# Performance work log

Measured on AMD Instinct MI355X. Metric: run time of the kernel, lower is better.

The kernel has to match this reference:

```python
import jax, jax.numpy as jnp
import numpy as np

K = 3          # deformable conv kernel size
DG = 4         # deformable groups
PAD = (K - 1) // 2


def _deform_conv(x, offset, w, dg=DG, pad=PAD):
    """DCNv1 forward (stride=1, dilation=1, conv groups=1, no bias).

    x:      [B, C, H, W]
    offset: [B, dg*K*K*2, H, W]  layout per group: (dy, dx) per kernel tap
    w:      [O, C, K, K]
    """
    B, C, H, W = x.shape
    O = w.shape[0]
    k2 = K * K
    gC = C // dg

    off = offset.reshape(B, dg, k2, 2, H, W)
    dy, dx = off[:, :, :, 0], off[:, :, :, 1]          # [B, dg, k2, H, W]

    ky, kx = jnp.meshgrid(jnp.arange(K), jnp.arange(K), indexing='ij')
    ky = ky.reshape(k2).astype(x.dtype)
    kx = kx.reshape(k2).astype(x.dtype)
    hi = jnp.arange(H, dtype=x.dtype)
    wi = jnp.arange(W, dtype=x.dtype)

    # absolute fractional sample coords: p0 - pad + kernel tap + learned offset
    ys = hi[None, None, None, :, None] - pad + ky[None, None, :, None, None] + dy
    xs = wi[None, None, None, None, :] - pad + kx[None, None, :, None, None] + dx

    y0 = jnp.floor(ys)
    x0 = jnp.floor(xs)
    ly = ys - y0   # bilinear weights
    lx = xs - x0
    y0 = y0.astype(jnp.int32)
    x0 = x0.astype(jnp.int32)

    xg = x.reshape(B, dg, gC, H * W)

    def gather(yi, xi):
        # zero padding outside the image (per-corner validity, matches mmcv)
        valid = ((yi >= 0) & (yi < H) & (xi >= 0) & (xi < W)).astype(x.dtype)
        idx = (jnp.clip(yi, 0, H - 1) * W + jnp.clip(xi, 0, W - 1)).reshape(B, dg, -1)
        vals = jax.vmap(jax.vmap(lambda t, i: t[:, i]))(xg, idx)  # [B,dg,gC,k2*H*W]
        return vals.reshape(B, dg, gC, k2, H, W) * valid[:, :, None]

    # bilinear interpolation of the 4 corners
    sampled = ((1 - ly) * (1 - lx))[:, :, None] * gather(y0,     x0) \
            + ((1 - ly) * lx      )[:, :, None] * gather(y0,     x0 + 1) \
            + (ly       * (1 - lx))[:, :, None] * gather(y0 + 1, x0) \
            + (ly       * lx      )[:, :, None] * gather(y0 + 1, x0 + 1)
    # sampled: [B, dg, gC, k2, H, W]

    wr = w.reshape(O, dg, gC, k2)
    return jnp.einsum('bgckhw,ogck->bohw', sampled, wr)


def setup_inputs() -> dict:
    key = jax.random.key(0)
    k0, k1, k2k, k3 = jax.random.split(key, 4)
    B, C, H, W, O = 2, 256, 128, 128, 256
    oc = DG * K * K * 2
    x = jax.random.normal(k0, (B, C, H, W), jnp.float32)
    # offset conv is zero-init in the module; use small random values so the
    # deformable sampling path is actually exercised
    w_offset = jax.random.normal(k1, (oc, C, 1, 1), jnp.float32) * 0.01
    b_offset = jax.random.normal(k2k, (oc,), jnp.float32) * 0.01
    w_deform = jax.random.normal(k3, (O, C, K, K), jnp.float32) / np.sqrt(C * K * K)
    return {"x": x, "w_offset": w_offset, "b_offset": b_offset, "w_deform": w_deform}


def reference(x, w_offset, b_offset, w_deform):
    # 1x1 conv predicting offsets
    offset = jnp.einsum('bchw,oc->bohw', x, w_offset[:, :, 0, 0]) \
             + b_offset[None, :, None, None]
    # deformable conv + ReLU
    return jax.nn.relu(_deform_conv(x, offset, w_deform))
```

## Files before the change

kernel.cpp:

```cpp
#include <hip/hip_runtime.h>

#define HW 16384

typedef __attribute__((ext_vector_type(4))) float f32x4;
typedef __attribute__((ext_vector_type(8))) short bf16x8;
typedef __attribute__((ext_vector_type(4))) int i32x4;

static __device__ __forceinline__ float bf2f(short s) {
    return __uint_as_float(((unsigned)(unsigned short)s) << 16);
}
static __device__ __forceinline__ unsigned short f2bf(float f) {
    unsigned u = __float_as_uint(f);
    unsigned r = u + 0x7fffu + ((u >> 16) & 1u);
    return (unsigned short)(r >> 16);
}
static __device__ __forceinline__ int cvt_pk_bf16(float lo, float hi) {
    int r;
    asm("v_cvt_pk_bf16_f32 %0, %1, %2" : "=v"(r) : "v"(lo), "v"(hi));
    return r;
}

__global__ __launch_bounds__(256) void prep_kernel(
    const float* __restrict__ x, const float* __restrict__ wd,
    const float* __restrict__ woff,
    unsigned short* __restrict__ xT, unsigned short* __restrict__ Wc2,
    unsigned short* __restrict__ Wo2)
{
    int bid = blockIdx.x;
    int tid = threadIdx.x;
    if (bid < 2048) {
        __shared__ float tl[64][65];
        int ct = bid & 3, pt = (bid >> 2) & 255, b = bid >> 10;
        const float* xb = x + ((size_t)(b * 256 + ct * 64)) * HW + pt * 64;
        #pragma unroll
        for (int j = 0; j < 4; ++j) {
            int slot = tid + j * 256;
            int c = slot >> 4, p4 = slot & 15;
            float4 v = *(const float4*)(xb + (size_t)c * HW + p4 * 4);
            tl[c][p4 * 4 + 0] = v.x;
            tl[c][p4 * 4 + 1] = v.y;
            tl[c][p4 * 4 + 2] = v.z;
            tl[c][p4 * 4 + 3] = v.w;
        }
        __syncthreads();
        unsigned short* ob = xT + ((size_t)(b * HW + pt * 64)) * 256 + ct * 64;
        #pragma unroll
        for (int j2 = 0; j2 < 2; ++j2) {
            int slot = tid + j2 * 256;
            int p = slot >> 3, sl = slot & 7;
            i32x4 st;
            #pragma unroll
            for (int kq = 0; kq < 4; ++kq)
                ((int*)&st)[kq] = cvt_pk_bf16(tl[sl*8 + kq*2][p], tl[sl*8 + kq*2 + 1][p]);
            *(i32x4*)(ob + (size_t)p * 256 + sl * 8) = st;
        }
    } else if (bid < 2336) {
        int slot = (bid - 2048) * 256 + tid;
        int l  = slot & 63;
        int ks = (slot >> 6) & 1;
        int mi = (slot >> 7) & 3;
        int q4 = (slot >> 9) & 3;
        int kc = slot >> 11;
        int g = kc / 9, tap = kc - g * 9;
        int o = q4 * 64 + mi * 16 + (l & 15);
        int cgb = (ks * 4 + (l >> 4)) * 8;
        unsigned short* dst = Wc2 + (size_t)slot * 8;
        const float* src = wd + (size_t)o * 2304 + tap;
        #pragma unroll
        for (int e = 0; e < 8; ++e)
            dst[e] = f2bf(src[(size_t)(g * 64 + cgb + e) * 9]);
    } else {
        int slot = (bid - 2336) * 256 + tid;
        int kk = slot / 320;
        int rem = slot - kk * 320;
        int o = rem >> 2, jq = rem & 3;
        unsigned short* dst = Wo2 + (size_t)slot * 8;
        #pragma unroll
        for (int e = 0; e < 8; ++e)
            dst[e] = (o < 72) ? f2bf(woff[(size_t)o * 256 + kk * 32 + jq * 8 + e]) : (unsigned short)0;
    }
}

__global__ __launch_bounds__(512, 4) void deform_kernel(
    const unsigned short* __restrict__ xT, const unsigned short* __restrict__ Wc2,
    const unsigned short* __restrict__ Wo2, const float* __restrict__ b_off,
    float* __restrict__ out)
{
    __shared__ int   c_yx[2304];
    __shared__ float c_ly[2304];
    __shared__ float c_lx[2304];
    __shared__ __align__(16) short Sbuf[2][4096];

    const int t    = threadIdx.x;
    const int lane = t & 63;
    const int q    = t >> 6;
    const int lr   = lane & 15, lq = lane >> 4;
    int bid = blockIdx.x;
    bid = (bid & 7) * 64 + (bid >> 3);
    const int gp0  = bid << 6;
    const int b    = gp0 >> 14;
    const int hw0  = gp0 & 16383;
    const int h    = hw0 >> 7;
    const int w0   = hw0 & 127;

    {
        const int p16 = (q & 3) * 16;
        bf16x8 xv[8];
        const unsigned short* xrow = xT + ((size_t)(b * HW + hw0 + p16 + lr)) * 256 + lq * 8;
        #pragma unroll
        for (int kk = 0; kk < 8; ++kk)
            xv[kk] = *(const bf16x8*)(xrow + kk * 32);
        const int mi0 = (q < 4) ? 0 : 3;
        const int nmi = (q < 4) ? 3 : 2;
        for (int im = 0; im < nmi; ++im) {
            int mi = mi0 + im;
            f32x4 oa = (f32x4)0.f;
            #pragma unroll
            for (int kk = 0; kk < 8; ++kk) {
                bf16x8 af = *(const bf16x8*)(Wo2 + (size_t)((kk * 80 + mi * 16 + lr) * 32 + lq * 8));
                oa = __builtin_amdgcn_mfma_f32_16x16x32_bf16(af, xv[kk], oa, 0, 0, 0);
            }
            #pragma unroll
            for (int ri = 0; ri < 2; ++ri) {
                int gt = mi * 8 + lq * 2 + ri;
                if (gt < 36) {
                    int p = p16 + lr;
                    float dy = oa[ri * 2]     + b_off[2 * gt];
                    float dx = oa[ri * 2 + 1] + b_off[2 * gt + 1];
                    int tap = gt % 9;
                    float ys = (float)(h - 1 + tap / 3) + dy;
                    float xs = (float)(w0 + p - 1 + tap % 3) + dx;
                    float fy = floorf(ys), fx = floorf(xs);
                    c_yx[gt * 64 + p] = ((int)fy & 0xffff) | ((int)fx << 16);
                    c_ly[gt * 64 + p] = ys - fy;
                    c_lx[gt * 64 + p] = xs - fx;
                }
            }
        }
    }
    __syncthreads();

    f32x4 acc[2][4];
    #pragma unroll
    for (int mi = 0; mi < 2; ++mi)
        #pragma unroll
        for (int nj = 0; nj < 4; ++nj)
            acc[mi][nj] = (f32x4)0.f;

    const unsigned short* xbase = xT + ((size_t)b * HW) * 256;
    const int ppix = q * 8 + (lane >> 3);
    const int sl   = lane & 7;
    const int q4   = q >> 1;
    const int mo   = (q & 1) * 2;

    {
        int idx = ppix;
        int yx = c_yx[idx];
        int y0 = (int)(short)(yx & 0xffff);
        int x0 = yx >> 16;
        float ly = c_ly[idx], lx = c_lx[idx];
        float omy = 1.f - ly, omx = 1.f - lx;
        float vy0 = ((unsigned)y0       < 128u) ? 1.f : 0.f;
        float vy1 = ((unsigned)(y0 + 1) < 128u) ? 1.f : 0.f;
        float vx0 = ((unsigned)x0       < 128u) ? 1.f : 0.f;
        float vx1 = ((unsigned)(x0 + 1) < 128u) ? 1.f : 0.f;
        float w00 = omy * omx * vy0 * vx0, w01 = omy * lx * vy0 * vx1;
        float w10 = ly  * omx * vy1 * vx0, w11 = ly  * lx * vy1 * vx1;
        int y0c = min(max(y0, 0), 127), y1c = min(max(y0 + 1, 0), 127);
        int x0c = min(max(x0, 0), 127), x1c = min(max(x0 + 1, 0), 127);
        const unsigned short* cb = xbase + (size_t)(sl * 8);
        bf16x8 v00 = *(const bf16x8*)(cb + (size_t)(y0c * 128 + x0c) * 256);
        bf16x8 v01 = *(const bf16x8*)(cb + (size_t)(y0c * 128 + x1c) * 256);
        bf16x8 v10 = *(const bf16x8*)(cb + (size_t)(y1c * 128 + x0c) * 256);
        bf16x8 v11 = *(const bf16x8*)(cb + (size_t)(y1c * 128 + x1c) * 256);
        float sv[8];
        #pragma unroll
        for (int e = 0; e < 8; ++e)
            sv[e] = w00 * bf2f(v00[e]) + w01 * bf2f(v01[e])
                  + w10 * bf2f(v10[e]) + w11 * bf2f(v11[e]);
        i32x4 st;
        #pragma unroll
        for (int kq = 0; kq < 4; ++kq)
            ((int*)&st)[kq] = cvt_pk_bf16(sv[kq * 2], sv[kq * 2 + 1]);
        ((i32x4*)Sbuf[0])[ppix * 8 + (sl ^ (ppix & 7))] = st;
    }
    __syncthreads();

    short* Sc = Sbuf[0];
    short* Sn = Sbuf[1];

    for (int kc = 0; kc < 36; ++kc) {
        bf16x8 v00, v01, v10, v11;
        float w00, w01, w10, w11;
        const bool pf = (kc < 35);
        if (pf) {
            int kn = kc + 1;
            int g  = kn / 9;
            int idx = kn * 64 + ppix;
            int yx = c_yx[idx];
            int y0 = (int)(short)(yx & 0xffff);
            int x0 = yx >> 16;
            float ly = c_ly[idx], lx = c_lx[idx];
            float omy = 1.f - ly, omx = 1.f - lx;
            float vy0 = ((unsigned)y0       < 128u) ? 1.f : 0.f;
            float vy1 = ((unsigned)(y0 + 1) < 128u) ? 1.f : 0.f;
            float vx0 = ((unsigned)x0       < 128u) ? 1.f : 0.f;
            float vx1 = ((unsigned)(x0 + 1) < 128u) ? 1.f : 0.f;
            w00 = omy * omx * vy0 * vx0; w01 = omy * lx * vy0 * vx1;
            w10 = ly  * omx * vy1 * vx0; w11 = ly  * lx * vy1 * vx1;
            int y0c = min(max(y0, 0), 127), y1c = min(max(y0 + 1, 0), 127);
            int x0c = min(max(x0, 0), 127), x1c = min(max(x0 + 1, 0), 127);
            const unsigned short* cb = xbase + (size_t)(g * 64 + sl * 8);
            v00 = *(const bf16x8*)(cb + (size_t)(y0c * 128 + x0c) * 256);
            v01 = *(const bf16x8*)(cb + (size_t)(y0c * 128 + x1c) * 256);
            v10 = *(const bf16x8*)(cb + (size_t)(y1c * 128 + x0c) * 256);
            v11 = *(const bf16x8*)(cb + (size_t)(y1c * 128 + x1c) * 256);
        }
        {
            bf16x8 a_[2][2];
            const unsigned short* wb = Wc2 + ((size_t)kc * 2048 + q4 * 512 + mo * 128 + lane) * 8;
            #pragma unroll
            for (int mi = 0; mi < 2; ++mi)
                #pragma unroll
                for (int ks = 0; ks < 2; ++ks)
                    a_[mi][ks] = *(const bf16x8*)(wb + (mi * 128 + ks * 64) * 8);
            #pragma unroll
            for (int ks = 0; ks < 2; ++ks) {
                bf16x8 bb[4];
                #pragma unroll
                for (int nj = 0; nj < 4; ++nj) {
                    int pp = nj * 16 + lr;
                    bb[nj] = *(const bf16x8*)&((const i32x4*)Sc)[pp * 8 + ((ks * 4 + lq) ^ (pp & 7))];
                }
                #pragma unroll
                for (int mi = 0; mi < 2; ++mi)
                    #pragma unroll
                    for (int nj = 0; nj < 4; ++nj)
                        acc[mi][nj] = __builtin_amdgcn_mfma_f32_16x16x32_bf16(
                            a_[mi][ks], bb[nj], acc[mi][nj], 0, 0, 0);
            }
        }
        if (pf) {
            float sv[8];
            #pragma unroll
            for (int e = 0; e < 8; ++e)
                sv[e] = w00 * bf2f(v00[e]) + w01 * bf2f(v01[e])
                      + w10 * bf2f(v10[e]) + w11 * bf2f(v11[e]);
            i32x4 st;
            #pragma unroll
            for (int kq = 0; kq < 4; ++kq)
                ((int*)&st)[kq] = cvt_pk_bf16(sv[kq * 2], sv[kq * 2 + 1]);
            ((i32x4*)Sn)[ppix * 8 + (sl ^ (ppix & 7))] = st;
        }
        __syncthreads();
        short* tmp = Sc; Sc = Sn; Sn = tmp;
    }

    #pragma unroll
    for (int mi = 0; mi < 2; ++mi)
        #pragma unroll
        for (int nj = 0; nj < 4; ++nj)
            #pragma unroll
            for (int r = 0; r < 4; ++r) {
                int o  = q * 32 + mi * 16 + lq * 4 + r;
                int pp = nj * 16 + lr;
                out[((size_t)(b * 256 + o) << 14) + hw0 + pp] = fmaxf(acc[mi][nj][r], 0.f);
            }
}

extern "C" void kernel_launch(void* const* d_in, const int* in_sizes, int n_in,
                              void* d_out, int out_size, void* d_ws, size_t ws_size,
                              hipStream_t stream) {
    const float* x     = (const float*)d_in[0];
    const float* w_off = (const float*)d_in[1];
    const float* b_off = (const float*)d_in[2];
    const float* w_def = (const float*)d_in[3];
    float* out = (float*)d_out;

    unsigned short* xT  = (unsigned short*)d_ws;
    unsigned short* Wc2 = (unsigned short*)((char*)d_ws + 16777216);
    unsigned short* Wo2 = (unsigned short*)((char*)d_ws + 17956864);

    prep_kernel<<<2346, 256, 0, stream>>>(x, w_def, w_off, xT, Wc2, Wo2);
    deform_kernel<<<512, 512, 0, stream>>>(xT, Wc2, Wo2, b_off, out);
}
```

Baseline: 162.4 us.

## Switch to fp16 storage and packed-half bilinear interpolation with precomputed corner weights

```diff
diff --git a/kernel.cpp b/kernel.cpp
--- a/kernel.cpp
+++ b/kernel.cpp
@@ -2,29 +2,26 @@
 
 #define HW 16384
 
+typedef _Float16 f16;
 typedef __attribute__((ext_vector_type(4))) float f32x4;
-typedef __attribute__((ext_vector_type(8))) short bf16x8;
+typedef __attribute__((ext_vector_type(8))) _Float16 f16x8;
 typedef __attribute__((ext_vector_type(4))) int i32x4;
 
-static __device__ __forceinline__ float bf2f(short s) {
-    return __uint_as_float(((unsigned)(unsigned short)s) << 16);
-}
-static __device__ __forceinline__ unsigned short f2bf(float f) {
-    unsigned u = __float_as_uint(f);
-    unsigned r = u + 0x7fffu + ((u >> 16) & 1u);
-    return (unsigned short)(r >> 16);
-}
-static __device__ __forceinline__ int cvt_pk_bf16(float lo, float hi) {
+union h8i4 { f16x8 h; i32x4 i; };
+
+static __device__ __forceinline__ int pk_f16(float lo, float hi) {
     int r;
-    asm("v_cvt_pk_bf16_f32 %0, %1, %2" : "=v"(r) : "v"(lo), "v"(hi));
+    asm("v_cvt_pkrtz_f16_f32 %0, %1, %2" : "=v"(r) : "v"(lo), "v"(hi));
     return r;
+}
+static __device__ __forceinline__ f16 ush2h(unsigned short u) {
+    union { unsigned short s; f16 h; } c; c.s = u; return c.h;
 }
 
 __global__ __launch_bounds__(256) void prep_kernel(
     const float* __restrict__ x, const float* __restrict__ wd,
     const float* __restrict__ woff,
-    unsigned short* __restrict__ xT, unsigned short* __restrict__ Wc2,
-    unsigned short* __restrict__ Wo2)
+    f16* __restrict__ xT, f16* __restrict__ Wc2, f16* __restrict__ Wo2)
 {
     int bid = blockIdx.x;
     int tid = threadIdx.x;
@@ -43,7 +40,7 @@
             tl[c][p4 * 4 + 3] = v.w;
         }
         __syncthreads();
-        unsigned short* ob = xT + ((size_t)(b * HW + pt * 64)) * 256 + ct * 64;
+        f16* ob = xT + ((size_t)(b * HW + pt * 64)) * 256 + ct * 64;
         #pragma unroll
         for (int j2 = 0; j2 < 2; ++j2) {
             int slot = tid + j2 * 256;
@@ -51,7 +48,7 @@
             i32x4 st;
             #pragma unroll
             for (int kq = 0; kq < 4; ++kq)
-                ((int*)&st)[kq] = cvt_pk_bf16(tl[sl*8 + kq*2][p], tl[sl*8 + kq*2 + 1][p]);
+                ((int*)&st)[kq] = pk_f16(tl[sl*8 + kq*2][p], tl[sl*8 + kq*2 + 1][p]);
             *(i32x4*)(ob + (size_t)p * 256 + sl * 8) = st;
         }
     } else if (bid < 2336) {
@@ -64,31 +61,29 @@
         int g = kc / 9, tap = kc - g * 9;
         int o = q4 * 64 + mi * 16 + (l & 15);
         int cgb = (ks * 4 + (l >> 4)) * 8;
-        unsigned short* dst = Wc2 + (size_t)slot * 8;
+        f16* dst = Wc2 + (size_t)slot * 8;
         const float* src = wd + (size_t)o * 2304 + tap;
         #pragma unroll
         for (int e = 0; e < 8; ++e)
-            dst[e] = f2bf(src[(size_t)(g * 64 + cgb + e) * 9]);
+            dst[e] = (f16)(src[(size_t)(g * 64 + cgb + e) * 9]);
     } else {
         int slot = (bid - 2336) * 256 + tid;
         int kk = slot / 320;
         int rem = slot - kk * 320;
         int o = rem >> 2, jq = rem & 3;
-        unsigned short* dst = Wo2 + (size_t)slot * 8;
+        f16* dst = Wo2 + (size_t)slot * 8;
         #pragma unroll
         for (int e = 0; e < 8; ++e)
-            dst[e] = (o < 72) ? f2bf(woff[(size_t)o * 256 + kk * 32 + jq * 8 + e]) : (unsigned short)0;
+            dst[e] = (o < 72) ? (f16)(woff[(size_t)o * 256 + kk * 32 + jq * 8 + e]) : (f16)0.f;
     }
 }
 
 __global__ __launch_bounds__(512, 4) void deform_kernel(
-    const unsigned short* __restrict__ xT, const unsigned short* __restrict__ Wc2,
-    const unsigned short* __restrict__ Wo2, const float* __restrict__ b_off,
+    const f16* __restrict__ xT, const f16* __restrict__ Wc2,
+    const f16* __restrict__ Wo2, const float* __restrict__ b_off,
     float* __restrict__ out)
 {
-    __shared__ int   c_yx[2304];
-    __shared__ float c_ly[2304];
-    __shared__ float c_lx[2304];
+    __shared__ __align__(16) i32x4 pk[2304];
     __shared__ __align__(16) short Sbuf[2][4096];
 
     const int t    = threadIdx.x;
@@ -105,11 +100,11 @@
 
     {
         const int p16 = (q & 3) * 16;
-        bf16x8 xv[8];
-        const unsigned short* xrow = xT + ((size_t)(b * HW + hw0 + p16 + lr)) * 256 + lq * 8;
+        f16x8 xv[8];
+        const f16* xrow = xT + ((size_t)(b * HW + hw0 + p16 + lr)) * 256 + lq * 8;
         #pragma unroll
         for (int kk = 0; kk < 8; ++kk)
-            xv[kk] = *(const bf16x8*)(xrow + kk * 32);
+            xv[kk] = *(const f16x8*)(xrow + kk * 32);
         const int mi0 = (q < 4) ? 0 : 3;
         const int nmi = (q < 4) ? 3 : 2;
         for (int im = 0; im < nmi; ++im) {
@@ -117,8 +112,8 @@
             f32x4 oa = (f32x4)0.f;
             #pragma unroll
             for (int kk = 0; kk < 8; ++kk) {
-                bf16x8 af = *(const bf16x8*)(Wo2 + (size_t)((kk * 80 + mi * 16 + lr) * 32 + lq * 8));
-                oa = __builtin_amdgcn_mfma_f32_16x16x32_bf16(af, xv[kk], oa, 0, 0, 0);
+                f16x8 af = *(const f16x8*)(Wo2 + (size_t)((kk * 80 + mi * 16 + lr) * 32 + lq * 8));
+                oa = __builtin_amdgcn_mfma_f32_16x16x32_f16(af, xv[kk], oa, 0, 0, 0);
             }
             #pragma unroll
             for (int ri = 0; ri < 2; ++ri) {
@@ -131,9 +126,21 @@
                     float ys = (float)(h - 1 + tap / 3) + dy;
                     float xs = (float)(w0 + p - 1 + tap % 3) + dx;
                     float fy = floorf(ys), fx = floorf(xs);
-                    c_yx[gt * 64 + p] = ((int)fy & 0xffff) | ((int)fx << 16);
-                    c_ly[gt * 64 + p] = ys - fy;
-                    c_lx[gt * 64 + p] = xs - fx;
+                    int y0 = (int)fy, x0 = (int)fx;
+                    float ly = ys - fy, lx = xs - fx;
+                    float omy = 1.f - ly, omx = 1.f - lx;
+                    float vy0 = ((unsigned)y0       < 128u) ? 1.f : 0.f;
+                    float vy1 = ((unsigned)(y0 + 1) < 128u) ? 1.f : 0.f;
+                    float vx0 = ((unsigned)x0       < 128u) ? 1.f : 0.f;
+                    float vx1 = ((unsigned)(x0 + 1) < 128u) ? 1.f : 0.f;
+                    int y0c = min(max(y0, 0), 127), y1c = min(max(y0 + 1, 0), 127);
+                    int x0c = min(max(x0, 0), 127), x1c = min(max(x0 + 1, 0), 127);
+                    i32x4 e;
+                    e.x = y0c * 128 + x0c;
+                    e.y = y1c * 128 + x1c;
+                    e.z = pk_f16(omy * omx * vy0 * vx0, omy * lx * vy0 * vx1);
+                    e.w = pk_f16(ly  * omx * vy1 * vx0, ly  * lx * vy1 * vx1);
+                    pk[gt * 64 + p] = e;
                 }
             }
         }
@@ -147,42 +154,28 @@
         for (int nj = 0; nj < 4; ++nj)
             acc[mi][nj] = (f32x4)0.f;
 
-    const unsigned short* xbase = xT + ((size_t)b * HW) * 256;
+    const f16* xbase = xT + ((size_t)b * HW) * 256;
     const int ppix = q * 8 + (lane >> 3);
     const int sl   = lane & 7;
     const int q4   = q >> 1;
     const int mo   = (q & 1) * 2;
 
     {
-        int idx = ppix;
-        int yx = c_yx[idx];
-        int y0 = (int)(short)(yx & 0xffff);
-        int x0 = yx >> 16;
-        float ly = c_ly[idx], lx = c_lx[idx];
-        float omy = 1.f - ly, omx = 1.f - lx;
-        float vy0 = ((unsigned)y0       < 128u) ? 1.f : 0.f;
-        float vy1 = ((unsigned)(y0 + 1) < 128u) ? 1.f : 0.f;
-        float vx0 = ((unsigned)x0       < 128u) ? 1.f : 0.f;
-        float vx1 = ((unsigned)(x0 + 1) < 128u) ? 1.f : 0.f;
-        float w00 = omy * omx * vy0 * vx0, w01 = omy * lx * vy0 * vx1;
-        float w10 = ly  * omx * vy1 * vx0, w11 = ly  * lx * vy1 * vx1;
-        int y0c = min(max(y0, 0), 127), y1c = min(max(y0 + 1, 0), 127);
-        int x0c = min(max(x0, 0), 127), x1c = min(max(x0 + 1, 0), 127);
-        const unsigned short* cb = xbase + (size_t)(sl * 8);
-        bf16x8 v00 = *(const bf16x8*)(cb + (size_t)(y0c * 128 + x0c) * 256);
-        bf16x8 v01 = *(const bf16x8*)(cb + (size_t)(y0c * 128 + x1c) * 256);
-        bf16x8 v10 = *(const bf16x8*)(cb + (size_t)(y1c * 128 + x0c) * 256);
-        bf16x8 v11 = *(const bf16x8*)(cb + (size_t)(y1c * 128 + x1c) * 256);
-        float sv[8];
-        #pragma unroll
-        for (int e = 0; e < 8; ++e)
-            sv[e] = w00 * bf2f(v00[e]) + w01 * bf2f(v01[e])
-                  + w10 * bf2f(v10[e]) + w11 * bf2f(v11[e]);
-        i32x4 st;
-        #pragma unroll
-        for (int kq = 0; kq < 4; ++kq)
-            ((int*)&st)[kq] = cvt_pk_bf16(sv[kq * 2], sv[kq * 2 + 1]);
-        ((i32x4*)Sbuf[0])[ppix * 8 + (sl ^ (ppix & 7))] = st;
+        i32x4 cd = pk[ppix];
+        int idx00 = cd.x, idx11 = cd.y;
+        int idx01 = (idx00 & ~127) | (idx11 & 127);
+        int idx10 = (idx11 & ~127) | (idx00 & 127);
+        f16x8 w00v = (f16x8)ush2h((unsigned short)(cd.z & 0xffff));
+        f16x8 w01v = (f16x8)ush2h((unsigned short)((unsigned)cd.z >> 16));
+        f16x8 w10v = (f16x8)ush2h((unsigned short)(cd.w & 0xffff));
+        f16x8 w11v = (f16x8)ush2h((unsigned short)((unsigned)cd.w >> 16));
+        const f16* cb = xbase + sl * 8;
+        f16x8 sv = *(const f16x8*)(cb + (size_t)idx00 * 256) * w00v;
+        sv += *(const f16x8*)(cb + (size_t)idx01 * 256) * w01v;
+        sv += *(const f16x8*)(cb + (size_t)idx10 * 256) * w10v;
+        sv += *(const f16x8*)(cb + (size_t)idx11 * 256) * w11v;
+        h8i4 u; u.h = sv;
+        ((i32x4*)Sbuf[0])[ppix * 8 + (sl ^ (ppix & 7))] = u.i;
     }
     __syncthreads();
 
@@ -190,67 +183,59 @@
     short* Sn = Sbuf[1];
 
     for (int kc = 0; kc < 36; ++kc) {
-        bf16x8 v00, v01, v10, v11;
-        float w00, w01, w10, w11;
+        f16x8 v00, v01, v10, v11;
+        f16x8 w00v, w01v, w10v, w11v;
         const bool pf = (kc < 35);
         if (pf) {
             int kn = kc + 1;
             int g  = kn / 9;
-            int idx = kn * 64 + ppix;
-            int yx = c_yx[idx];
-            int y0 = (int)(short)(yx & 0xffff);
-            int x0 = yx >> 16;
-            float ly = c_ly[idx], lx = c_lx[idx];
-            float omy = 1.f - ly, omx = 1.f - lx;
-            float vy0 = ((unsigned)y0       < 128u) ? 1.f : 0.f;
-            float vy1 = ((unsigned)(y0 + 1) < 128u) ? 1.f : 0.f;
-            float vx0 = ((unsigned)x0       < 128u) ? 1.f : 0.f;
-            float vx1 = ((unsigned)(x0 + 1) < 128u) ? 1.f : 0.f;
-            w00 = omy * omx * vy0 * vx0; w01 = omy * lx * vy0 * vx1;
-            w10 = ly  * omx * vy1 * vx0; w11 = ly  * lx * vy1 * vx1;
-            int y0c = min(max(y0, 0), 127), y1c = min(max(y0 + 1, 0), 127);
-            int x0c = min(max(x0, 0), 127), x1c = min(max(x0 + 1, 0), 127);
-            const unsigned short* cb = xbase + (size_t)(g * 64 + sl * 8);
-            v00 = *(const bf16x8*)(cb + (size_t)(y0c * 128 + x0c) * 256);
-            v01 = *(const bf16x8*)(cb + (size_t)(y0c * 128 + x1c) * 256);
-            v10 = *(const bf16x8*)(cb + (size_t)(y1c * 128 + x0c) * 256);
-            v11 = *(const bf16x8*)(cb + (size_t)(y1c * 128 + x1c) * 256);
+            i32x4 cd = pk[kn * 64 + ppix];
+            int idx00 = cd.x, idx11 = cd.y;
+            int idx01 = (idx00 & ~127) | (idx11 & 127);
+            int idx10 = (idx11 & ~127) | (idx00 & 127);
+            w00v = (f16x8)ush2h((unsigned short)(cd.z & 0xffff));
+            w01v = (f16x8)ush2h((unsigned short)((unsigned)cd.z >> 16));
+            w10v = (f16x8)ush2h((unsigned short)(cd.w & 0xffff));
+            w11v = (f16x8)ush2h((unsigned short)((unsigned)cd.w >> 16));
+            const f16* cb = xbase + (size_t)(g * 64 + sl * 8);
+            v00 = *(const f16x8*)(cb + (size_t)idx00 * 256);
+            v01 = *(const f16x8*)(cb + (size_t)idx01 * 256);
+            v10 = *(const f16x8*)(cb + (size_t)idx10 * 256);
+            v11 = *(const f16x8*)(cb + (size_t)idx11 * 256);
         }
         {
-            bf16x8 a_[2][2];
-            const unsigned short* wb = Wc2 + ((size_t)kc * 2048 + q4 * 512 + mo * 128 + lane) * 8;
+            f16x8 a_[2][2];
+            const f16* wb = Wc2 + ((size_t)kc * 2048 + q4 * 512 + mo * 128 + lane) * 8;
             #pragma unroll
             for (int mi = 0; mi < 2; ++mi)
                 #pragma unroll
                 for (int ks = 0; ks < 2; ++ks)
-                    a_[mi][ks] = *(const bf16x8*)(wb + (mi * 128 + ks * 64) * 8);
+                    a_[mi][ks] = *(const f16x8*)(wb + (mi * 128 + ks * 64) * 8);
             #pragma unroll
             for (int ks = 0; ks < 2; ++ks) {
-                bf16x8 bb[4];
+                f16x8 bb[4];
                 #pragma unroll
                 for (int nj = 0; nj < 4; ++nj) {
                     int pp = nj * 16 + lr;
-                    bb[nj] = *(const bf16x8*)&((const i32x4*)Sc)[pp * 8 + ((ks * 4 + lq) ^ (pp & 7))];
+                    h8i4 u;
+                    u.i = ((const i32x4*)Sc)[pp * 8 + ((ks * 4 + lq) ^ (pp & 7))];
+                    bb[nj] = u.h;
                 }
                 #pragma unroll
                 for (int mi = 0; mi < 2; ++mi)
                     #pragma unroll
                     for (int nj = 0; nj < 4; ++nj)
-                        acc[mi][nj] = __builtin_amdgcn_mfma_f32_16x16x32_bf16(
+                        acc[mi][nj] = __builtin_amdgcn_mfma_f32_16x16x32_f16(
                             a_[mi][ks], bb[nj], acc[mi][nj], 0, 0, 0);
             }
         }
         if (pf) {
-            float sv[8];
-            #pragma unroll
-            for (int e = 0; e < 8; ++e)
-                sv[e] = w00 * bf2f(v00[e]) + w01 * bf2f(v01[e])
-                      + w10 * bf2f(v10[e]) + w11 * bf2f(v11[e]);
-            i32x4 st;
-            #pragma unroll
-            for (int kq = 0; kq < 4; ++kq)
-                ((int*)&st)[kq] = cvt_pk_bf16(sv[kq * 2], sv[kq * 2 + 1]);
-            ((i32x4*)Sn)[ppix * 8 + (sl ^ (ppix & 7))] = st;
+            f16x8 sv = v00 * w00v;
+            sv += v01 * w01v;
+            sv += v10 * w10v;
+            sv += v11 * w11v;
+            h8i4 u; u.h = sv;
+            ((i32x4*)Sn)[ppix * 8 + (sl ^ (ppix & 7))] = u.i;
         }
         __syncthreads();
         short* tmp = Sc; Sc = Sn; Sn = tmp;
@@ -277,9 +262,9 @@
     const float* w_def = (const float*)d_in[3];
     float* out = (float*)d_out;
 
-    unsigned short* xT  = (unsigned short*)d_ws;
-    unsigned short* Wc2 = (unsigned short*)((char*)d_ws + 16777216);
-    unsigned short* Wo2 = (unsigned short*)((char*)d_ws + 17956864);
+    f16* xT  = (f16*)d_ws;
+    f16* Wc2 = (f16*)((char*)d_ws + 16777216);
+    f16* Wo2 = (f16*)((char*)d_ws + 17956864);
 
     prep_kernel<<<2346, 256, 0, stream>>>(x, w_def, w_off, xT, Wc2, Wo2);
     deform_kernel<<<512, 512, 0, stream>>>(xT, Wc2, Wo2, b_off, out);
```

Result: faster. 148.5 us (-8.6%).
